# Kernel tuning notes

Measured on AMD Instinct MI355X. Metric: run time of the kernel, lower is better.

Reference implementation:

```python
import jax, jax.numpy as jnp
import numpy as np

K = 5          # k = min(5, min(S, T)) with S = T = 4096
SIGMA = 1.0
EPS_VAR = 1e-08
EPS_LOG = 1e-08


def _entropy(p):
    # sum(-p * log2(clamp(p, 1e-8)), axis=1).mean()
    return jnp.sum(-p * jnp.log2(jnp.clip(p, EPS_LOG, None)), axis=1).mean()


def _pairwise_dist(x):
    # Euclidean cdist via GEMM (matches torch's use_mm_for_euclid path)
    sq = jnp.sum(x * x, axis=1)                       # [N]
    d2 = sq[:, None] + sq[None, :] - 2.0 * (x @ x.T)  # [N, N]
    d2 = jnp.maximum(d2, 0.0)
    # safe sqrt (zero diagonal) — value identical, grad-safe
    return jnp.where(d2 > 0, jnp.sqrt(jnp.where(d2 > 0, d2, 1.0)), 0.0)


def _row_var(block):
    # sqrt(k-th smallest distance per row + eps): max of k smallest
    kth = -jax.lax.top_k(-block, K)[0][:, -1]
    return jnp.sqrt(kth + EPS_VAR)                    # [rows]


def _sim(block, var_row, zero_diag):
    s = jnp.exp(-block / (2.0 * (var_row[:, None] * SIGMA) ** 2))
    if zero_diag:
        n = block.shape[0]
        s = s * (1.0 - jnp.eye(n, dtype=s.dtype))
    return s


def _forward(Feature_all, logit_all, y_source):
    S = y_source.shape[0]
    logit_source = logit_all[:S]
    logit_target = logit_all[S:]

    # cross-entropy on source
    logp = jax.nn.log_softmax(logit_source, axis=1)
    loss_cl = -jnp.take_along_axis(logp, y_source[:, None], axis=1).mean()

    # entropy of target softmax
    loss_ce = _entropy(jax.nn.softmax(logit_target, axis=1))

    # reg_loss_dist
    dist = _pairwise_dist(Feature_all)                # [N, N]
    d_ss = dist[:S, :S]
    d_st = dist[:S, S:]
    d_tt = dist[S:, S:]
    d_ts = dist[S:, :S]

    sim_ss = _sim(d_ss, _row_var(d_ss), True)
    sim_st = _sim(d_st, _row_var(d_st), False)
    sim_tt = _sim(d_tt, _row_var(d_tt), True)
    sim_ts = _sim(d_ts, _row_var(d_ts), False)

    src_intra = jnp.max(sim_ss, axis=1)
    src_inter = jnp.max(sim_st, axis=1)
    tgt_intra = jnp.max(sim_tt, axis=1)
    tgt_inter = jnp.max(sim_ts, axis=1)

    loss_reg = (jnp.abs(src_intra - src_inter).mean()
                + jnp.abs(tgt_intra - tgt_inter).mean())
    return loss_cl, loss_ce, loss_reg


def setup_inputs() -> dict:
    key = jax.random.key(0)
    k1, k2, k3 = jax.random.split(key, 3)
    N, D, C, S = 8192, 256, 65, 4096
    return {
        "Feature_all": jax.random.normal(k1, (N, D), dtype=jnp.float32),
        "logit_all": jax.random.normal(k2, (N, C), dtype=jnp.float32),
        "y_source": jax.random.randint(k3, (S,), 0, C, dtype=jnp.int64
                                       if jax.config.jax_enable_x64 else jnp.int32),
        "device": 0,
    }


def reference(Feature_all, logit_all, y_source, device):
    del device  # torch-specific, ignored
    return _forward(Feature_all, logit_all, y_source)
```

## Files before the change

### kernel.cpp

```cpp
#include <hip/hip_runtime.h>
#include <stdint.h>

#define Nn 8192
#define Dd 256
#define Ss 4096
#define Cc 65

#define TI 128
#define TJ 128
#define BK 32
#define CHUNK 1024
#define NCHUNK (Nn / CHUNK)
#define NJT (CHUNK / TJ)
#define KS (Dd / BK)

#define BIGF 3.0e37f

typedef float f4 __attribute__((ext_vector_type(4)));
typedef __bf16 bf8 __attribute__((ext_vector_type(8)));

__device__ __forceinline__ float wredsum(float v) {
#pragma unroll
  for (int o = 32; o; o >>= 1) v += __shfl_xor(v, o, 64);
  return v;
}
__device__ __forceinline__ float wredmax(float v) {
#pragma unroll
  for (int o = 32; o; o >>= 1) v = fmaxf(v, __shfl_xor(v, o, 64));
  return v;
}

__device__ __forceinline__ unsigned short f2bf(float f) {
  unsigned int u = __float_as_uint(f);
  u = (u + 0x7fffu + ((u >> 16) & 1u)) >> 16;
  return (unsigned short)u;
}

__global__ __launch_bounds__(256) void prep_kernel(const float* __restrict__ X,
                                                   unsigned short* __restrict__ xb,
                                                   float* __restrict__ sqn) {
  int row = blockIdx.x * 4 + (threadIdx.x >> 6);
  int lane = threadIdx.x & 63;
  f4 v = ((const f4*)(X + (size_t)row * Dd))[lane];
  float ss = v[0] * v[0] + v[1] * v[1] + v[2] * v[2] + v[3] * v[3];
  ss = wredsum(ss);
  if (lane == 0) sqn[row] = ss;
  ushort4 o;
  o.x = f2bf(v[0]); o.y = f2bf(v[1]); o.z = f2bf(v[2]); o.w = f2bf(v[3]);
  ((ushort4*)(xb + (size_t)row * Dd))[lane] = o;
}

__device__ __forceinline__ void stage16(const void* g, void* l) {
  __builtin_amdgcn_global_load_lds((__attribute__((address_space(1))) void*)g,
                                   (__attribute__((address_space(3))) void*)l, 16, 0, 0);
}

__global__ __launch_bounds__(256) void dist_kernel(const unsigned short* __restrict__ xb,
                                                   const float* __restrict__ sqn,
                                                   float* __restrict__ top5ws) {
  __shared__ unsigned short ldsA[2][TJ * BK];
  __shared__ unsigned short ldsB[2][TI * BK];

  const int tid = threadIdx.x;
  const int lane = tid & 63;
  const int wv = tid >> 6;
  const int q = lane >> 4;
  const int c = lane & 15;
  const int jw = wv & 1;
  const int iw = wv >> 1;

  const int ib = (blockIdx.x / NCHUNK) * TI;
  const int chunk = blockIdx.x % NCHUNK;
  const int jc0 = chunk * CHUNK;

  const int swz = q ^ ((lane >> 1) & 3);
  const int pr = lane >> 2;
  const int qd = (lane & 3) ^ ((lane >> 3) & 3);
  const int u0 = wv * 2, u1 = wv * 2 + 1;
  const int gcol = qd * 8;

  float top[4][5];
#pragma unroll
  for (int a = 0; a < 4; ++a)
#pragma unroll
    for (int b = 0; b < 5; ++b) top[a][b] = BIGF;

  const int iwbase = ib + iw * 64;

  for (int jt = 0; jt < NJT; ++jt) {
    const int jb = jc0 + jt * TJ;

    f4 acc[4][4];
    f4 z = {0.f, 0.f, 0.f, 0.f};
#pragma unroll
    for (int a = 0; a < 4; ++a)
#pragma unroll
      for (int b2 = 0; b2 < 4; ++b2) acc[a][b2] = z;

    stage16(xb + (size_t)(jb + u0 * 16 + pr) * Dd + gcol, &ldsA[0][u0 * 512]);
    stage16(xb + (size_t)(jb + u1 * 16 + pr) * Dd + gcol, &ldsA[0][u1 * 512]);
    stage16(xb + (size_t)(ib + u0 * 16 + pr) * Dd + gcol, &ldsB[0][u0 * 512]);
    stage16(xb + (size_t)(ib + u1 * 16 + pr) * Dd + gcol, &ldsB[0][u1 * 512]);
    __syncthreads();

#pragma unroll
    for (int ks = 0; ks < KS; ++ks) {
      const int b = ks & 1;
      if (ks + 1 < KS) {
        const int k0 = (ks + 1) * BK;
        stage16(xb + (size_t)(jb + u0 * 16 + pr) * Dd + k0 + gcol, &ldsA[b ^ 1][u0 * 512]);
        stage16(xb + (size_t)(jb + u1 * 16 + pr) * Dd + k0 + gcol, &ldsA[b ^ 1][u1 * 512]);
        stage16(xb + (size_t)(ib + u0 * 16 + pr) * Dd + k0 + gcol, &ldsB[b ^ 1][u0 * 512]);
        stage16(xb + (size_t)(ib + u1 * 16 + pr) * Dd + k0 + gcol, &ldsB[b ^ 1][u1 * 512]);
      }
      bf8 aF[4], bF[4];
#pragma unroll
      for (int rt = 0; rt < 4; ++rt)
        aF[rt] = *(const bf8*)&ldsA[b][(jw * 64 + rt * 16 + c) * 32 + swz * 8];
#pragma unroll
      for (int ct = 0; ct < 4; ++ct)
        bF[ct] = *(const bf8*)&ldsB[b][(iw * 64 + ct * 16 + c) * 32 + swz * 8];
#pragma unroll
      for (int rt = 0; rt < 4; ++rt)
#pragma unroll
        for (int ct = 0; ct < 4; ++ct)
          acc[rt][ct] = __builtin_amdgcn_mfma_f32_16x16x32_bf16(aF[rt], bF[ct], acc[rt][ct], 0, 0, 0);
      __syncthreads();
    }

    const int jrow = jb + jw * 64;
    f4 sq4[4];
#pragma unroll
    for (int rt = 0; rt < 4; ++rt) sq4[rt] = *(const f4*)&sqn[jrow + rt * 16 + q * 4];
    const bool mayDiag = (jrow == iwbase);
#pragma unroll
    for (int ct = 0; ct < 4; ++ct) {
      float t[16];
#pragma unroll
      for (int rt = 0; rt < 4; ++rt)
#pragma unroll
        for (int r = 0; r < 4; ++r)
          t[rt * 4 + r] = fmaf(acc[rt][ct][r], -2.0f, sq4[rt][r]);
      if (mayDiag && ((c >> 2) == q)) t[ct * 4 + (c & 3)] = BIGF;
      float tm = fminf(fminf(fminf(fminf(t[0], t[1]), fminf(t[2], t[3])),
                             fminf(fminf(t[4], t[5]), fminf(t[6], t[7]))),
                       fminf(fminf(fminf(t[8], t[9]), fminf(t[10], t[11])),
                             fminf(fminf(t[12], t[13]), fminf(t[14], t[15]))));
      if (tm < top[ct][4]) {
#pragma unroll
        for (int kk = 0; kk < 16; ++kk) {
          float x = t[kk];
          if (x < top[ct][4]) {
#pragma unroll
            for (int s = 0; s < 4; ++s) {
              float lo = fminf(top[ct][s], x);
              x = fmaxf(top[ct][s], x);
              top[ct][s] = lo;
            }
            top[ct][4] = x;
          }
        }
      }
    }
  }

#pragma unroll
  for (int ct = 0; ct < 4; ++ct) {
    float a0 = top[ct][0], a1 = top[ct][1], a2 = top[ct][2], a3 = top[ct][3], a4 = top[ct][4];
#pragma unroll
    for (int off = 16; off <= 32; off <<= 1) {
      float b0 = __shfl_xor(a0, off, 64);
      float b1 = __shfl_xor(a1, off, 64);
      float b2 = __shfl_xor(a2, off, 64);
      float b3 = __shfl_xor(a3, off, 64);
      float b4 = __shfl_xor(a4, off, 64);
      float c0 = fminf(a0, b0);
      float c1 = fminf(fminf(a1, b1), fmaxf(a0, b0));
      float c2 = fminf(fminf(a2, b2), fminf(fmaxf(a1, b0), fmaxf(a0, b1)));
      float c3 = fminf(fminf(a3, b3), fminf(fmaxf(a2, b0), fminf(fmaxf(a1, b1), fmaxf(a0, b2))));
      float c4 = fminf(fminf(a4, b4),
                       fminf(fmaxf(a3, b0),
                             fminf(fmaxf(a2, b1), fminf(fmaxf(a1, b2), fmaxf(a0, b3)))));
      a0 = c0; a1 = c1; a2 = c2; a3 = c3; a4 = c4;
    }
    if (q == 0) {
      int i = iwbase + ct * 16 + c;
      float* dst = top5ws + ((size_t)i * (NCHUNK * 2) + (chunk * 2 + jw)) * 5;
      dst[0] = a0; dst[1] = a1; dst[2] = a2; dst[3] = a3; dst[4] = a4;
    }
  }
}

__device__ __forceinline__ void merge5(const float* a, const float* b, float* o) {
  o[0] = fminf(a[0], b[0]);
  o[1] = fminf(fminf(a[1], b[1]), fmaxf(a[0], b[0]));
  o[2] = fminf(fminf(a[2], b[2]), fminf(fmaxf(a[1], b[0]), fmaxf(a[0], b[1])));
  o[3] = fminf(fminf(a[3], b[3]), fminf(fmaxf(a[2], b[0]), fminf(fmaxf(a[1], b[1]), fmaxf(a[0], b[2]))));
  o[4] = fminf(fminf(a[4], b[4]),
               fminf(fmaxf(a[3], b[0]),
                     fminf(fmaxf(a[2], b[1]), fminf(fmaxf(a[1], b[2]), fmaxf(a[0], b[3])))));
}

__device__ __forceinline__ void merge8lists(const float* L, float* o) {
  float m01[5], m23[5], m45[5], m67[5], mA[5], mB[5];
  merge5(L + 0, L + 5, m01);
  merge5(L + 10, L + 15, m23);
  merge5(L + 20, L + 25, m45);
  merge5(L + 30, L + 35, m67);
  merge5(m01, m23, mA);
  merge5(m45, m67, mB);
  merge5(mA, mB, o);
}

__global__ __launch_bounds__(256) void reg_kernel(const float* __restrict__ top5ws,
                                                  const float* __restrict__ sqn,
                                                  float* __restrict__ part_reg) {
  int i = blockIdx.x * 256 + threadIdx.x;
  float buf[80];
  const float* L = top5ws + (size_t)i * 80;
#pragma unroll
  for (int k = 0; k < 80; ++k) buf[k] = L[k];
  float mlo[5], mhi[5];
  merge8lists(buf, mlo);
  merge8lists(buf + 40, mhi);
  bool srcRow = (i < Ss);
  float A0 = srcRow ? mlo[0] : mhi[0];
  float A3 = srcRow ? mlo[3] : mhi[3];
  float B0 = srcRow ? mhi[0] : mlo[0];
  float B4 = srcRow ? mhi[4] : mlo[4];
  float sq = sqn[i];
  float dmin_a = sqrtf(fmaxf(A0 + sq, 0.f));
  float kth_a = sqrtf(fmaxf(A3 + sq, 0.f));
  float dmin_b = sqrtf(fmaxf(B0 + sq, 0.f));
  float kth_b = sqrtf(fmaxf(B4 + sq, 0.f));
  float sa = expf(-dmin_a / (2.f * (kth_a + 1e-8f)));
  float sb = expf(-dmin_b / (2.f * (kth_b + 1e-8f)));
  float v = fabsf(sa - sb);
  __shared__ float red[256];
  red[threadIdx.x] = v;
  __syncthreads();
#pragma unroll
  for (int s = 128; s; s >>= 1) {
    if (threadIdx.x < s) red[threadIdx.x] += red[threadIdx.x + s];
    __syncthreads();
  }
  if (threadIdx.x == 0) part_reg[blockIdx.x] = red[0];
}

__global__ __launch_bounds__(256) void loss_kernel(const float* __restrict__ logit,
                                                   const int* __restrict__ y,
                                                   float* __restrict__ part_cl,
                                                   float* __restrict__ part_ce) {
  int row = blockIdx.x * 4 + (threadIdx.x >> 6);
  int lane = threadIdx.x & 63;
  const float* xr = logit + (size_t)row * Cc;
  float x1 = xr[lane];
  float x2 = (lane == 0) ? xr[64] : -BIGF;
  float mx = wredmax(fmaxf(x1, x2));
  float e1 = expf(x1 - mx);
  float e2 = (lane == 0) ? expf(x2 - mx) : 0.f;
  float Z = wredsum(e1 + e2);
  float res;
  if (row < Ss) {
    int yy = y[row];
    float pick = (lane == yy ? x1 : 0.f) + ((lane == 0 && yy == 64) ? x2 : 0.f);
    float xy = wredsum(pick);
    res = -(xy - mx - logf(Z));
  } else {
    float p1 = e1 / Z;
    float t1 = -p1 * log2f(fmaxf(p1, 1e-8f));
    if (lane == 0) {
      float p2 = e2 / Z;
      t1 += -p2 * log2f(fmaxf(p2, 1e-8f));
    }
    res = wredsum(t1);
  }
  __shared__ float a4[4];
  if (lane == 0) a4[threadIdx.x >> 6] = res;
  __syncthreads();
  if (threadIdx.x == 0) {
    float s = a4[0] + a4[1] + a4[2] + a4[3];
    if (blockIdx.x < 1024) part_cl[blockIdx.x] = s;
    else part_ce[blockIdx.x - 1024] = s;
  }
}

__global__ __launch_bounds__(256) void final_kernel(const float* __restrict__ part_cl,
                                                    const float* __restrict__ part_ce,
                                                    const float* __restrict__ part_reg,
                                                    float* __restrict__ out) {
  __shared__ double red[256];
  int tid = threadIdx.x;
  double a = 0.0;
  for (int k = tid; k < 1024; k += 256) a += (double)part_cl[k];
  red[tid] = a; __syncthreads();
  for (int s = 128; s; s >>= 1) { if (tid < s) red[tid] += red[tid + s]; __syncthreads(); }
  double cl = red[0]; __syncthreads();
  a = 0.0;
  for (int k = tid; k < 1024; k += 256) a += (double)part_ce[k];
  red[tid] = a; __syncthreads();
  for (int s = 128; s; s >>= 1) { if (tid < s) red[tid] += red[tid + s]; __syncthreads(); }
  double ce = red[0]; __syncthreads();
  a = (tid < 16) ? (double)part_reg[tid] : 0.0;
  red[tid] = a; __syncthreads();
  for (int s = 128; s; s >>= 1) { if (tid < s) red[tid] += red[tid + s]; __syncthreads(); }
  double rs = red[0]; __syncthreads();
  a = (tid >= 16 && tid < 32) ? (double)part_reg[tid] : 0.0;
  red[tid] = a; __syncthreads();
  for (int s = 128; s; s >>= 1) { if (tid < s) red[tid] += red[tid + s]; __syncthreads(); }
  if (tid == 0) {
    out[0] = (float)(cl / 4096.0);
    out[1] = (float)(ce / 4096.0);
    out[2] = (float)(rs / 4096.0 + red[0] / 4096.0);
  }
}

extern "C" void kernel_launch(void* const* d_in, const int* in_sizes, int n_in,
                              void* d_out, int out_size, void* d_ws, size_t ws_size,
                              hipStream_t stream) {
  (void)in_sizes; (void)n_in; (void)out_size; (void)ws_size;
  const float* X = (const float*)d_in[0];
  const float* logit = (const float*)d_in[1];
  const int* y = (const int*)d_in[2];
  float* out = (float*)d_out;
  char* ws = (char*)d_ws;

  unsigned short* xb = (unsigned short*)ws;
  float* sqn = (float*)(ws + (4u << 20));
  float* top5 = (float*)(ws + (4u << 20) + (64u << 10));
  float* part_cl = (float*)(ws + (7u << 20));
  float* part_ce = part_cl + 1024;
  float* part_reg = part_ce + 1024;

  hipLaunchKernelGGL(prep_kernel, dim3(2048), dim3(256), 0, stream, X, xb, sqn);
  hipLaunchKernelGGL(dist_kernel, dim3((Nn / TI) * NCHUNK), dim3(256), 0, stream, xb, sqn, top5);
  hipLaunchKernelGGL(reg_kernel, dim3(32), dim3(256), 0, stream, top5, sqn, part_reg);
  hipLaunchKernelGGL(loss_kernel, dim3(2048), dim3(256), 0, stream, logit, y, part_cl, part_ce);
  hipLaunchKernelGGL(final_kernel, dim3(1), dim3(256), 0, stream, part_cl, part_ce, part_reg, out);
}
```

Baseline: 154.1 us.

## Fuse prep with loss, merge final into reg via atomic counter, halve chunk

```diff
diff --git a/kernel.cpp b/kernel.cpp
--- a/kernel.cpp
+++ b/kernel.cpp
@@ -9,7 +9,7 @@
 #define TI 128
 #define TJ 128
 #define BK 32
-#define CHUNK 1024
+#define CHUNK 512
 #define NCHUNK (Nn / CHUNK)
 #define NJT (CHUNK / TJ)
 #define KS (Dd / BK)
@@ -36,18 +36,69 @@
   return (unsigned short)u;
 }
 
-__global__ __launch_bounds__(256) void prep_kernel(const float* __restrict__ X,
-                                                   unsigned short* __restrict__ xb,
-                                                   float* __restrict__ sqn) {
-  int row = blockIdx.x * 4 + (threadIdx.x >> 6);
+__device__ __forceinline__ void merge5(const float* a, const float* b, float* o) {
+  o[0] = fminf(a[0], b[0]);
+  o[1] = fminf(fminf(a[1], b[1]), fmaxf(a[0], b[0]));
+  o[2] = fminf(fminf(a[2], b[2]), fminf(fmaxf(a[1], b[0]), fmaxf(a[0], b[1])));
+  o[3] = fminf(fminf(a[3], b[3]), fminf(fmaxf(a[2], b[0]), fminf(fmaxf(a[1], b[1]), fmaxf(a[0], b[2]))));
+  o[4] = fminf(fminf(a[4], b[4]),
+               fminf(fmaxf(a[3], b[0]),
+                     fminf(fmaxf(a[2], b[1]), fminf(fmaxf(a[1], b[2]), fmaxf(a[0], b[3])))));
+}
+
+__global__ __launch_bounds__(256) void prep_loss_kernel(const float* __restrict__ X,
+                                                        unsigned short* __restrict__ xb,
+                                                        float* __restrict__ sqn,
+                                                        const float* __restrict__ logit,
+                                                        const int* __restrict__ y,
+                                                        float* __restrict__ part_cl,
+                                                        float* __restrict__ part_ce,
+                                                        unsigned int* __restrict__ counter) {
+  if (blockIdx.x == 0 && threadIdx.x == 0) *counter = 0u;
   int lane = threadIdx.x & 63;
-  f4 v = ((const f4*)(X + (size_t)row * Dd))[lane];
-  float ss = v[0] * v[0] + v[1] * v[1] + v[2] * v[2] + v[3] * v[3];
-  ss = wredsum(ss);
-  if (lane == 0) sqn[row] = ss;
-  ushort4 o;
-  o.x = f2bf(v[0]); o.y = f2bf(v[1]); o.z = f2bf(v[2]); o.w = f2bf(v[3]);
-  ((ushort4*)(xb + (size_t)row * Dd))[lane] = o;
+  if (blockIdx.x < 2048) {
+    int row = blockIdx.x * 4 + (threadIdx.x >> 6);
+    f4 v = ((const f4*)(X + (size_t)row * Dd))[lane];
+    float ss = v[0] * v[0] + v[1] * v[1] + v[2] * v[2] + v[3] * v[3];
+    ss = wredsum(ss);
+    if (lane == 0) sqn[row] = ss;
+    ushort4 o;
+    o.x = f2bf(v[0]); o.y = f2bf(v[1]); o.z = f2bf(v[2]); o.w = f2bf(v[3]);
+    ((ushort4*)(xb + (size_t)row * Dd))[lane] = o;
+  } else {
+    int bid = blockIdx.x - 2048;
+    int row = bid * 4 + (threadIdx.x >> 6);
+    const float* xr = logit + (size_t)row * Cc;
+    float x1 = xr[lane];
+    float x2 = (lane == 0) ? xr[64] : -BIGF;
+    float mx = wredmax(fmaxf(x1, x2));
+    float e1 = expf(x1 - mx);
+    float e2 = (lane == 0) ? expf(x2 - mx) : 0.f;
+    float Z = wredsum(e1 + e2);
+    float res;
+    if (row < Ss) {
+      int yy = y[row];
+      float pick = (lane == yy ? x1 : 0.f) + ((lane == 0 && yy == 64) ? x2 : 0.f);
+      float xy = wredsum(pick);
+      res = -(xy - mx - logf(Z));
+    } else {
+      float p1 = e1 / Z;
+      float t1 = -p1 * log2f(fmaxf(p1, 1e-8f));
+      if (lane == 0) {
+        float p2 = e2 / Z;
+        t1 += -p2 * log2f(fmaxf(p2, 1e-8f));
+      }
+      res = wredsum(t1);
+    }
+    __shared__ float a4[4];
+    if (lane == 0) a4[threadIdx.x >> 6] = res;
+    __syncthreads();
+    if (threadIdx.x == 0) {
+      float s = a4[0] + a4[1] + a4[2] + a4[3];
+      if (bid < 1024) part_cl[bid] = s;
+      else part_ce[bid - 1024] = s;
+    }
+  }
 }
 
 __device__ __forceinline__ void stage16(const void* g, void* l) {
@@ -164,6 +215,7 @@
     }
   }
 
+  float fin[4][5];
 #pragma unroll
   for (int ct = 0; ct < 4; ++ct) {
     float a0 = top[ct][0], a1 = top[ct][1], a2 = top[ct][2], a3 = top[ct][3], a4 = top[ct][4];
@@ -183,22 +235,30 @@
                              fminf(fmaxf(a2, b1), fminf(fmaxf(a1, b2), fmaxf(a0, b3)))));
       a0 = c0; a1 = c1; a2 = c2; a3 = c3; a4 = c4;
     }
-    if (q == 0) {
+    fin[ct][0] = a0; fin[ct][1] = a1; fin[ct][2] = a2; fin[ct][3] = a3; fin[ct][4] = a4;
+  }
+
+  float* mbuf = (float*)ldsA;
+  if (jw == 1 && q == 0) {
+#pragma unroll
+    for (int ct = 0; ct < 4; ++ct) {
+      float* m = mbuf + ((((iw << 2) | ct) << 4) + c) * 5;
+      m[0] = fin[ct][0]; m[1] = fin[ct][1]; m[2] = fin[ct][2]; m[3] = fin[ct][3]; m[4] = fin[ct][4];
+    }
+  }
+  __syncthreads();
+  if (jw == 0 && q == 0) {
+#pragma unroll
+    for (int ct = 0; ct < 4; ++ct) {
+      const float* m = mbuf + ((((iw << 2) | ct) << 4) + c) * 5;
+      float bl[5] = {m[0], m[1], m[2], m[3], m[4]};
+      float o[5];
+      merge5(fin[ct], bl, o);
       int i = iwbase + ct * 16 + c;
-      float* dst = top5ws + ((size_t)i * (NCHUNK * 2) + (chunk * 2 + jw)) * 5;
-      dst[0] = a0; dst[1] = a1; dst[2] = a2; dst[3] = a3; dst[4] = a4;
-    }
-  }
-}
-
-__device__ __forceinline__ void merge5(const float* a, const float* b, float* o) {
-  o[0] = fminf(a[0], b[0]);
-  o[1] = fminf(fminf(a[1], b[1]), fmaxf(a[0], b[0]));
-  o[2] = fminf(fminf(a[2], b[2]), fminf(fmaxf(a[1], b[0]), fmaxf(a[0], b[1])));
-  o[3] = fminf(fminf(a[3], b[3]), fminf(fmaxf(a[2], b[0]), fminf(fmaxf(a[1], b[1]), fmaxf(a[0], b[2]))));
-  o[4] = fminf(fminf(a[4], b[4]),
-               fminf(fmaxf(a[3], b[0]),
-                     fminf(fmaxf(a[2], b[1]), fminf(fmaxf(a[1], b[2]), fmaxf(a[0], b[3])))));
+      float* dst = top5ws + ((size_t)i * NCHUNK + chunk) * 5;
+      dst[0] = o[0]; dst[1] = o[1]; dst[2] = o[2]; dst[3] = o[3]; dst[4] = o[4];
+    }
+  }
 }
 
 __device__ __forceinline__ void merge8lists(const float* L, float* o) {
@@ -212,9 +272,13 @@
   merge5(mA, mB, o);
 }
 
-__global__ __launch_bounds__(256) void reg_kernel(const float* __restrict__ top5ws,
-                                                  const float* __restrict__ sqn,
-                                                  float* __restrict__ part_reg) {
+__global__ __launch_bounds__(256) void reg_final_kernel(const float* __restrict__ top5ws,
+                                                        const float* __restrict__ sqn,
+                                                        float* __restrict__ part_reg,
+                                                        const float* __restrict__ part_cl,
+                                                        const float* __restrict__ part_ce,
+                                                        float* __restrict__ out,
+                                                        unsigned int* __restrict__ counter) {
   int i = blockIdx.x * 256 + threadIdx.x;
   float buf[80];
   const float* L = top5ws + (size_t)i * 80;
@@ -245,73 +309,37 @@
     __syncthreads();
   }
   if (threadIdx.x == 0) part_reg[blockIdx.x] = red[0];
-}
-
-__global__ __launch_bounds__(256) void loss_kernel(const float* __restrict__ logit,
-                                                   const int* __restrict__ y,
-                                                   float* __restrict__ part_cl,
-                                                   float* __restrict__ part_ce) {
-  int row = blockIdx.x * 4 + (threadIdx.x >> 6);
-  int lane = threadIdx.x & 63;
-  const float* xr = logit + (size_t)row * Cc;
-  float x1 = xr[lane];
-  float x2 = (lane == 0) ? xr[64] : -BIGF;
-  float mx = wredmax(fmaxf(x1, x2));
-  float e1 = expf(x1 - mx);
-  float e2 = (lane == 0) ? expf(x2 - mx) : 0.f;
-  float Z = wredsum(e1 + e2);
-  float res;
-  if (row < Ss) {
-    int yy = y[row];
-    float pick = (lane == yy ? x1 : 0.f) + ((lane == 0 && yy == 64) ? x2 : 0.f);
-    float xy = wredsum(pick);
-    res = -(xy - mx - logf(Z));
-  } else {
-    float p1 = e1 / Z;
-    float t1 = -p1 * log2f(fmaxf(p1, 1e-8f));
-    if (lane == 0) {
-      float p2 = e2 / Z;
-      t1 += -p2 * log2f(fmaxf(p2, 1e-8f));
-    }
-    res = wredsum(t1);
-  }
-  __shared__ float a4[4];
-  if (lane == 0) a4[threadIdx.x >> 6] = res;
+
+  __shared__ unsigned int lastFlag;
+  __threadfence();
+  if (threadIdx.x == 0) lastFlag = (atomicAdd(counter, 1u) == 31u) ? 1u : 0u;
   __syncthreads();
-  if (threadIdx.x == 0) {
-    float s = a4[0] + a4[1] + a4[2] + a4[3];
-    if (blockIdx.x < 1024) part_cl[blockIdx.x] = s;
-    else part_ce[blockIdx.x - 1024] = s;
-  }
-}
-
-__global__ __launch_bounds__(256) void final_kernel(const float* __restrict__ part_cl,
-                                                    const float* __restrict__ part_ce,
-                                                    const float* __restrict__ part_reg,
-                                                    float* __restrict__ out) {
-  __shared__ double red[256];
+  if (!lastFlag) return;
+  __threadfence();
+
+  __shared__ double dred[256];
   int tid = threadIdx.x;
   double a = 0.0;
   for (int k = tid; k < 1024; k += 256) a += (double)part_cl[k];
-  red[tid] = a; __syncthreads();
-  for (int s = 128; s; s >>= 1) { if (tid < s) red[tid] += red[tid + s]; __syncthreads(); }
-  double cl = red[0]; __syncthreads();
+  dred[tid] = a; __syncthreads();
+  for (int s = 128; s; s >>= 1) { if (tid < s) dred[tid] += dred[tid + s]; __syncthreads(); }
+  double cl = dred[0]; __syncthreads();
   a = 0.0;
   for (int k = tid; k < 1024; k += 256) a += (double)part_ce[k];
-  red[tid] = a; __syncthreads();
-  for (int s = 128; s; s >>= 1) { if (tid < s) red[tid] += red[tid + s]; __syncthreads(); }
-  double ce = red[0]; __syncthreads();
+  dred[tid] = a; __syncthreads();
+  for (int s = 128; s; s >>= 1) { if (tid < s) dred[tid] += dred[tid + s]; __syncthreads(); }
+  double ce = dred[0]; __syncthreads();
   a = (tid < 16) ? (double)part_reg[tid] : 0.0;
-  red[tid] = a; __syncthreads();
-  for (int s = 128; s; s >>= 1) { if (tid < s) red[tid] += red[tid + s]; __syncthreads(); }
-  double rs = red[0]; __syncthreads();
+  dred[tid] = a; __syncthreads();
+  for (int s = 128; s; s >>= 1) { if (tid < s) dred[tid] += dred[tid + s]; __syncthreads(); }
+  double rs = dred[0]; __syncthreads();
   a = (tid >= 16 && tid < 32) ? (double)part_reg[tid] : 0.0;
-  red[tid] = a; __syncthreads();
-  for (int s = 128; s; s >>= 1) { if (tid < s) red[tid] += red[tid + s]; __syncthreads(); }
+  dred[tid] = a; __syncthreads();
+  for (int s = 128; s; s >>= 1) { if (tid < s) dred[tid] += dred[tid + s]; __syncthreads(); }
   if (tid == 0) {
     out[0] = (float)(cl / 4096.0);
     out[1] = (float)(ce / 4096.0);
-    out[2] = (float)(rs / 4096.0 + red[0] / 4096.0);
+    out[2] = (float)(rs / 4096.0 + dred[0] / 4096.0);
   }
 }
 
@@ -331,10 +359,11 @@
   float* part_cl = (float*)(ws + (7u << 20));
   float* part_ce = part_cl + 1024;
   float* part_reg = part_ce + 1024;
-
-  hipLaunchKernelGGL(prep_kernel, dim3(2048), dim3(256), 0, stream, X, xb, sqn);
+  unsigned int* counter = (unsigned int*)(part_reg + 32);
+
+  hipLaunchKernelGGL(prep_loss_kernel, dim3(4096), dim3(256), 0, stream, X, xb, sqn, logit, y,
+                     part_cl, part_ce, counter);
   hipLaunchKernelGGL(dist_kernel, dim3((Nn / TI) * NCHUNK), dim3(256), 0, stream, xb, sqn, top5);
-  hipLaunchKernelGGL(reg_kernel, dim3(32), dim3(256), 0, stream, top5, sqn, part_reg);
-  hipLaunchKernelGGL(loss_kernel, dim3(2048), dim3(256), 0, stream, logit, y, part_cl, part_ce);
-  hipLaunchKernelGGL(final_kernel, dim3(1), dim3(256), 0, stream, part_cl, part_ce, part_reg, out);
-}
+  hipLaunchKernelGGL(reg_final_kernel, dim3(32), dim3(256), 0, stream, top5, sqn, part_reg,
+                     part_cl, part_ce, out, counter);
+}
```

New measurement: 156.5 us. Within noise of the previous version (+1.5%).
